# Performance work log

Hardware: AMD Instinct MI355X
Metric: run time of the kernel (lower is better)

## Reference

```python
import jax, jax.numpy as jnp
import numpy as np

# Dims: N tokens, D input, H expert hidden, O output, E experts, G gate hidden, K top-k
N, D, H, O, E, G, K = 8192, 1024, 2048, 1024, 8, 256, 2
BALANCE_COEF = 0.01


def setup_inputs() -> dict:
    key = jax.random.key(0)
    ks = jax.random.split(key, 12)
    def lin(k, shape, fan_in):
        return jax.random.normal(k, shape, jnp.float32) * (1.0 / np.sqrt(fan_in))
    return {
        "x":   jax.random.normal(ks[0], (N, D), jnp.float32),
        # gating MLP: D -> G -> E
        "Wg1": lin(ks[1], (D, G), D), "bg1": jnp.zeros((G,), jnp.float32),
        "Wg2": lin(ks[2], (G, E), G), "bg2": jnp.zeros((E,), jnp.float32),
        # stacked expert MLPs: D -> H -> H -> O (ExpertNetwork, num_layers=2)
        "W1": lin(ks[3], (E, D, H), D), "b1": jnp.zeros((E, H), jnp.float32),
        "W2": lin(ks[4], (E, H, H), H), "b2": jnp.zeros((E, H), jnp.float32),
        "W3": lin(ks[5], (E, H, O), H), "b3": jnp.zeros((E, O), jnp.float32),
    }


def reference(x, Wg1, bg1, Wg2, bg2, W1, b1, W2, b2, W3, b3):
    # Gating: 2-layer MLP -> softmax -> top-k -> renormalize (eval: no noise/dropout)
    logits = jnp.maximum(x @ Wg1 + bg1, 0.0) @ Wg2 + bg2            # [N, E]
    probs = jax.nn.softmax(logits, axis=-1)
    w, idx = jax.lax.top_k(probs, K)                                # [N, K]
    w = w / jnp.sum(w, axis=-1, keepdims=True)
    onehot = jax.nn.one_hot(idx, E, dtype=x.dtype)                  # [N, K, E]
    comb = jnp.sum(onehot * w[..., None], axis=1)                   # [N, E] per-token expert weight

    # Dense-equivalent combine: unselected tokens get weight 0, identical math to
    # the masked dispatch + scatter-add in the torch code.
    def expert_step(acc, params):
        W1e, b1e, W2e, b2e, W3e, b3e, we = params                   # we: [N]
        h = jnp.maximum(x @ W1e + b1e, 0.0)                         # [N, H]
        h = jnp.maximum(h @ W2e + b2e, 0.0)                         # [N, H]
        o = h @ W3e + b3e                                           # [N, O]
        return acc + o * we[:, None], None

    out, _ = jax.lax.scan(expert_step, jnp.zeros((N, O), x.dtype),
                          (W1, b1, W2, b2, W3, b3, comb.T))

    # aux losses: expert_usage[e] = sum_i mean_b(indices[b,i]==e)
    expert_usage = jnp.sum(onehot, axis=(0, 1)) / N                 # [E]
    balance_loss = jnp.mean((expert_usage - 1.0 / E) ** 2) * BALANCE_COEF
    return out, balance_loss, expert_usage
```

## Files before the change

### kernel.cpp

```cpp
#include <hip/hip_runtime.h>
#include <hip/hip_bf16.h>
#include <cstdint>
#include <cstddef>

#define N_TOK 8192
#define D_IN  1024
#define H_DIM 2048
#define O_DIM 1024
#define E_NUM 8
#define G_DIM 256
#define MAXTILES 136
#define MAXROWS  (MAXTILES*128)

typedef __attribute__((ext_vector_type(8))) __bf16 bf16x8;
typedef __attribute__((ext_vector_type(4))) __bf16 bf16x4;
typedef __attribute__((ext_vector_type(4))) float floatx4;

#define GCAST(p) ((__attribute__((address_space(1))) void*)(void*)(p))
#define LCAST(p) ((__attribute__((address_space(3))) void*)(p))

#define JOB_G1_END   512
#define JOB_CAST_END 4608
#define JOB_W1_END   8704
#define JOB_W2_END   16896
#define JOB_W3_END   20992

__device__ inline void transpose_body(const float* __restrict__ src,
                                      __bf16* __restrict__ dst,
                                      int K, int N, int e, int ktile, int ntile,
                                      float* smemf) {
  float (*tl)[68] = (float(*)[68])smemf;
  const float* s = src + (size_t)e * K * N;
  __bf16* d = dst + (size_t)e * K * N;
  int k0 = ktile * 64, n0 = ntile * 64;
  int t = threadIdx.x;
  int kr = t >> 4, nc = t & 15;
#pragma unroll
  for (int p = 0; p < 4; p++) {
    float4 v = *reinterpret_cast<const float4*>(
        s + (size_t)(k0 + kr + p * 16) * N + n0 + nc * 4);
    *reinterpret_cast<float4*>(&tl[kr + p * 16][nc * 4]) = v;
  }
  __syncthreads();
  int n = t >> 2, kg = t & 3;
#pragma unroll
  for (int p = 0; p < 2; p++) {
    bf16x8 o;
#pragma unroll
    for (int j = 0; j < 8; j++) o[j] = (__bf16)tl[p * 32 + kg * 8 + j][n];
    *reinterpret_cast<bf16x8*>(d + (size_t)(n0 + n) * K + k0 + p * 32 + kg * 8) = o;
  }
}

__device__ inline void gate1_body(const float* __restrict__ x,
                                  const float* __restrict__ Wg1,
                                  const float* __restrict__ bg1,
                                  float* __restrict__ g,
                                  int bn, int bm, float* smemf) {
  float (*As)[68] = (float(*)[68])smemf;
  float (*Bs)[68] = (float(*)[68])(smemf + 32 * 68);
  int t = threadIdx.x;
  int tm = t >> 4, tn = t & 15;
  float acc[4][4] = {};
  for (int k0 = 0; k0 < D_IN; k0 += 32) {
#pragma unroll
    for (int i = 0; i < 2; i++) {
      int idx = t + 256 * i;
      int row = idx >> 3, c4 = idx & 7;
      float4 v = *reinterpret_cast<const float4*>(
          x + (size_t)(bm * 64 + row) * D_IN + k0 + c4 * 4);
      As[c4 * 4 + 0][row] = v.x;
      As[c4 * 4 + 1][row] = v.y;
      As[c4 * 4 + 2][row] = v.z;
      As[c4 * 4 + 3][row] = v.w;
      int brow = idx >> 4, bc4 = idx & 15;
      float4 wv = *reinterpret_cast<const float4*>(
          Wg1 + (size_t)(k0 + brow) * G_DIM + bn * 64 + bc4 * 4);
      *reinterpret_cast<float4*>(&Bs[brow][bc4 * 4]) = wv;
    }
    __syncthreads();
#pragma unroll
    for (int k = 0; k < 32; k++) {
      float4 av = *reinterpret_cast<const float4*>(&As[k][tm * 4]);
      float4 bv = *reinterpret_cast<const float4*>(&Bs[k][tn * 4]);
      float a4[4] = {av.x, av.y, av.z, av.w};
      float b4[4] = {bv.x, bv.y, bv.z, bv.w};
#pragma unroll
      for (int r = 0; r < 4; r++)
#pragma unroll
        for (int c = 0; c < 4; c++) acc[r][c] = fmaf(a4[r], b4[c], acc[r][c]);
    }
    __syncthreads();
  }
  int gr = bm * 64 + tm * 4, gc = bn * 64 + tn * 4;
#pragma unroll
  for (int r = 0; r < 4; r++) {
    float4 o;
    o.x = fmaxf(acc[r][0] + bg1[gc + 0], 0.f);
    o.y = fmaxf(acc[r][1] + bg1[gc + 1], 0.f);
    o.z = fmaxf(acc[r][2] + bg1[gc + 2], 0.f);
    o.w = fmaxf(acc[r][3] + bg1[gc + 3], 0.f);
    *reinterpret_cast<float4*>(g + (size_t)(gr + r) * G_DIM + gc) = o;
  }
}

__global__ __launch_bounds__(256) void prep_kernel(
    const float* __restrict__ x, __bf16* __restrict__ xb,
    const float* __restrict__ W1, __bf16* __restrict__ W1t,
    const float* __restrict__ W2, __bf16* __restrict__ W2t,
    const float* __restrict__ W3, __bf16* __restrict__ W3t,
    const float* __restrict__ Wg1, const float* __restrict__ bg1,
    float* __restrict__ g) {
  __shared__ float smemf[4352];
  int b = blockIdx.x;
  if (b < JOB_G1_END) {
    gate1_body(x, Wg1, bg1, g, b & 3, b >> 2, smemf);
  } else if (b < JOB_CAST_END) {
    int id = b - JOB_G1_END;
    int i = id * 2048 + threadIdx.x * 8;
    float4 v0 = *reinterpret_cast<const float4*>(x + i);
    float4 v1 = *reinterpret_cast<const float4*>(x + i + 4);
    bf16x8 o;
    o[0] = (__bf16)v0.x; o[1] = (__bf16)v0.y; o[2] = (__bf16)v0.z; o[3] = (__bf16)v0.w;
    o[4] = (__bf16)v1.x; o[5] = (__bf16)v1.y; o[6] = (__bf16)v1.z; o[7] = (__bf16)v1.w;
    *reinterpret_cast<bf16x8*>(xb + i) = o;
  } else if (b < JOB_W1_END) {
    int id = b - JOB_CAST_END;
    transpose_body(W1, W1t, D_IN, H_DIM, id >> 9, (id >> 5) & 15, id & 31, smemf);
  } else if (b < JOB_W2_END) {
    int id = b - JOB_W1_END;
    transpose_body(W2, W2t, H_DIM, H_DIM, id >> 10, (id >> 5) & 31, id & 31, smemf);
  } else {
    int id = b - JOB_W2_END;
    transpose_body(W3, W3t, H_DIM, O_DIM, id >> 9, (id >> 4) & 31, id & 15, smemf);
  }
}

__global__ __launch_bounds__(256) void gate2_kernel(const float* __restrict__ g,
                                                    const float* __restrict__ Wg2,
                                                    const float* __restrict__ bg2,
                                                    int* __restrict__ top_idx,
                                                    float* __restrict__ top_w,
                                                    int* __restrict__ counts) {
  __shared__ float lg[32][9];
  int t = threadIdx.x;
  int tl = t >> 3, e = t & 7;
  int n = blockIdx.x * 32 + tl;
  const float* gr = g + (size_t)n * G_DIM;
  float acc = bg2[e];
  for (int i = 0; i < G_DIM; i += 4) {
    float4 v = *reinterpret_cast<const float4*>(gr + i);
    acc += v.x * Wg2[(i + 0) * E_NUM + e];
    acc += v.y * Wg2[(i + 1) * E_NUM + e];
    acc += v.z * Wg2[(i + 2) * E_NUM + e];
    acc += v.w * Wg2[(i + 3) * E_NUM + e];
  }
  lg[tl][e] = acc;
  __syncthreads();
  if (e == 0) {
    float l[8];
#pragma unroll
    for (int i = 0; i < 8; i++) l[i] = lg[tl][i];
    int i0 = 0;
    for (int i = 1; i < 8; i++)
      if (l[i] > l[i0]) i0 = i;
    int i1 = (i0 == 0) ? 1 : 0;
    for (int i = 0; i < 8; i++)
      if (i != i0 && l[i] > l[i1]) i1 = i;
    float d = expf(l[i1] - l[i0]);
    float w0 = 1.f / (1.f + d);
    float w1 = d * w0;
    top_idx[n * 2 + 0] = i0;
    top_idx[n * 2 + 1] = i1;
    top_w[n * 2 + 0] = w0;
    top_w[n * 2 + 1] = w1;
    atomicAdd(&counts[i0], 1);
    atomicAdd(&counts[i1], 1);
  }
}

__global__ void g3_kernel(const int* __restrict__ counts, int* __restrict__ cursors,
                          int* __restrict__ off_pad, int* __restrict__ ntiles,
                          int* __restrict__ tile_meta, float* __restrict__ out_tail,
                          int* __restrict__ slot_token) {
  if (threadIdx.x == 0) {
    int off = 0, nt = 0;
    float mse = 0.f;
    for (int e = 0; e < E_NUM; e++) {
      off_pad[e] = off;
      int c = counts[e];
      int tiles = (c + 127) >> 7;
      for (int i = 0; i < tiles; i++) {
        tile_meta[nt * 2 + 0] = e;
        tile_meta[nt * 2 + 1] = off + i * 128;
        nt++;
      }
      off += tiles << 7;
      cursors[e] = 0;
      float u = (float)c / (float)N_TOK;
      out_tail[1 + e] = u;
      float dd = u - 0.125f;
      mse += dd * dd;
    }
    *ntiles = nt;
    out_tail[0] = (mse / 8.0f) * 0.01f;
  }
  for (int s = threadIdx.x; s < MAXROWS; s += 256) slot_token[s] = 0;
}

__global__ __launch_bounds__(256) void scatter_kernel(const int* __restrict__ top_idx,
                                                      const int* __restrict__ off_pad,
                                                      int* __restrict__ cursors,
                                                      int* __restrict__ slot_token,
                                                      int* __restrict__ token_slots) {
  int n = blockIdx.x * 256 + threadIdx.x;
#pragma unroll
  for (int k = 0; k < 2; k++) {
    int e = top_idx[n * 2 + k];
    int pos = atomicAdd(&cursors[e], 1);
    int s = off_pad[e] + pos;
    slot_token[s] = n;
    token_slots[n * 2 + k] = s;
  }
}

__global__ __launch_bounds__(256) void moe_gemm_kernel(
    const __bf16* __restrict__ A, int Astride, int gatherA,
    const __bf16* __restrict__ Wt, const float* __restrict__ bias,
    int Kdim, int Ndim,
    const int* __restrict__ tile_meta, const int* __restrict__ ntiles_p,
    const int* __restrict__ slot_token,
    __bf16* __restrict__ h_out, float* __restrict__ y_out, int finalMode) {
  int tile = blockIdx.y;
  if (tile >= *ntiles_p) return;
  __shared__ __bf16 As[128 * 32];
  __shared__ __bf16 Bs[128 * 32];
  int ex = tile_meta[tile * 2 + 0];
  int slot0 = tile_meta[tile * 2 + 1];
  int n0 = blockIdx.x * 128;
  int t = threadIdx.x, l = t & 63, w = t >> 6;

  size_t aoff[2], boff[2];
#pragma unroll
  for (int i = 0; i < 2; i++) {
    int gidx = (w * 2 + i) * 64 + l;
    int row = gidx >> 2;
    int kch = (gidx & 3) ^ ((row >> 1) & 3);
    int sl = slot0 + row;
    long long rb = gatherA ? (long long)slot_token[sl] * Astride
                           : (long long)sl * Astride;
    aoff[i] = (size_t)rb + kch * 8;
    boff[i] = ((size_t)ex * Ndim + n0 + row) * (size_t)Kdim + kch * 8;
  }

  int wm = (w >> 1) * 64, wn = (w & 1) * 64;
  int lm = l & 15, lq = l >> 4;
  floatx4 acc[4][4] = {};

  for (int k0 = 0; k0 < Kdim; k0 += 32) {
#pragma unroll
    for (int i = 0; i < 2; i++) {
      __builtin_amdgcn_global_load_lds(GCAST(A + aoff[i] + k0),
                                       LCAST((char*)As + w * 2048 + i * 1024),
                                       16, 0, 0);
      __builtin_amdgcn_global_load_lds(GCAST(Wt + boff[i] + k0),
                                       LCAST((char*)Bs + w * 2048 + i * 1024),
                                       16, 0, 0);
    }
    __syncthreads();
    bf16x8 af[4], bfr[4];
#pragma unroll
    for (int i = 0; i < 4; i++) {
      int r = wm + i * 16 + lm;
      int s = lq ^ ((r >> 1) & 3);
      af[i] = *reinterpret_cast<const bf16x8*>(As + r * 32 + s * 8);
    }
#pragma unroll
    for (int j = 0; j < 4; j++) {
      int r = wn + j * 16 + lm;
      int s = lq ^ ((r >> 1) & 3);
      bfr[j] = *reinterpret_cast<const bf16x8*>(Bs + r * 32 + s * 8);
    }
#pragma unroll
    for (int i = 0; i < 4; i++)
#pragma unroll
      for (int j = 0; j < 4; j++)
        acc[i][j] = __builtin_amdgcn_mfma_f32_16x16x32_bf16(af[i], bfr[j], acc[i][j], 0, 0, 0);
    __syncthreads();
  }

  float bcol[4];
#pragma unroll
  for (int j = 0; j < 4; j++) bcol[j] = bias[(size_t)ex * Ndim + n0 + wn + j * 16 + lm];

  if (finalMode) {
#pragma unroll
    for (int i = 0; i < 4; i++) {
#pragma unroll
      for (int r = 0; r < 4; r++) {
        int sl = slot0 + wm + i * 16 + lq * 4 + r;
        float* yrow = y_out + (size_t)sl * Ndim + n0 + wn + lm;
#pragma unroll
        for (int j = 0; j < 4; j++) yrow[j * 16] = acc[i][j][r] + bcol[j];
      }
    }
  } else {
#pragma unroll
    for (int i = 0; i < 4; i++) {
#pragma unroll
      for (int r = 0; r < 4; r++) {
        int sl = slot0 + wm + i * 16 + lq * 4 + r;
        __bf16* hrow = h_out + (size_t)sl * Ndim + n0 + wn + lm;
#pragma unroll
        for (int j = 0; j < 4; j++) {
          float v = fmaxf(acc[i][j][r] + bcol[j], 0.f);
          hrow[j * 16] = (__bf16)v;
        }
      }
    }
  }
}

__global__ __launch_bounds__(256) void combine_kernel(const float* __restrict__ y,
                                                      const int* __restrict__ token_slots,
                                                      const float* __restrict__ top_w,
                                                      float* __restrict__ out) {
  int n = blockIdx.x;
  int t = threadIdx.x;
  int s0 = token_slots[n * 2 + 0], s1 = token_slots[n * 2 + 1];
  float w0 = top_w[n * 2 + 0], w1 = top_w[n * 2 + 1];
  float4 a = reinterpret_cast<const float4*>(y + (size_t)s0 * O_DIM)[t];
  float4 b = reinterpret_cast<const float4*>(y + (size_t)s1 * O_DIM)[t];
  float4 o;
  o.x = w0 * a.x + w1 * b.x;
  o.y = w0 * a.y + w1 * b.y;
  o.z = w0 * a.z + w1 * b.z;
  o.w = w0 * a.w + w1 * b.w;
  reinterpret_cast<float4*>(out + (size_t)n * O_DIM)[t] = o;
}

extern "C" void kernel_launch(void* const* d_in, const int* in_sizes, int n_in,
                              void* d_out, int out_size, void* d_ws, size_t ws_size,
                              hipStream_t stream) {
  const float* x   = (const float*)d_in[0];
  const float* Wg1 = (const float*)d_in[1];
  const float* bg1 = (const float*)d_in[2];
  const float* Wg2 = (const float*)d_in[3];
  const float* bg2 = (const float*)d_in[4];
  const float* W1  = (const float*)d_in[5];
  const float* b1  = (const float*)d_in[6];
  const float* W2  = (const float*)d_in[7];
  const float* b2  = (const float*)d_in[8];
  const float* W3  = (const float*)d_in[9];
  const float* b3  = (const float*)d_in[10];
  float* out = (float*)d_out;

  char* ws = (char*)d_ws;
  __bf16* x_bf       = (__bf16*)(ws + 0);
  __bf16* W1t        = (__bf16*)(ws + 16777216);
  __bf16* W2t        = (__bf16*)(ws + 50331648);
  __bf16* W3t        = (__bf16*)(ws + 117440512);
  __bf16* h1         = (__bf16*)(ws + 150994944);
  __bf16* h2         = (__bf16*)(ws + 222298112);
  float*  y          = (float*) (ws + 150994944);
  float*  gbuf       = (float*) (ws + 293601280);
  int*    top_idx    = (int*)   (ws + 301989888);
  float*  top_w      = (float*) (ws + 302055424);
  int*    slot_token = (int*)   (ws + 302120960);
  int*    token_slots= (int*)   (ws + 302190592);
  int*    meta       = (int*)   (ws + 302260224);
  int* counts    = meta;
  int* cursors   = meta + 8;
  int* off_pad   = meta + 16;
  int* ntiles    = meta + 24;
  int* tile_meta = meta + 32;
  float* out_tail = out + (size_t)N_TOK * O_DIM;

  hipMemsetAsync(meta, 0, 64, stream);

  prep_kernel<<<JOB_W3_END, 256, 0, stream>>>(x, x_bf, W1, W1t, W2, W2t, W3, W3t,
                                              Wg1, bg1, gbuf);
  gate2_kernel<<<N_TOK / 32, 256, 0, stream>>>(gbuf, Wg2, bg2, top_idx, top_w, counts);
  g3_kernel<<<1, 256, 0, stream>>>(counts, cursors, off_pad, ntiles, tile_meta, out_tail,
                                   slot_token);
  scatter_kernel<<<N_TOK / 256, 256, 0, stream>>>(top_idx, off_pad, cursors,
                                                  slot_token, token_slots);

  moe_gemm_kernel<<<dim3(H_DIM / 128, MAXTILES), 256, 0, stream>>>(
      x_bf, D_IN, 1, W1t, b1, D_IN, H_DIM, tile_meta, ntiles, slot_token,
      h1, nullptr, 0);
  moe_gemm_kernel<<<dim3(H_DIM / 128, MAXTILES), 256, 0, stream>>>(
      h1, H_DIM, 0, W2t, b2, H_DIM, H_DIM, tile_meta, ntiles, slot_token,
      h2, nullptr, 0);
  moe_gemm_kernel<<<dim3(O_DIM / 128, MAXTILES), 256, 0, stream>>>(
      h2, H_DIM, 0, W3t, b3, H_DIM, O_DIM, tile_meta, ntiles, slot_token,
      nullptr, y, 1);
  combine_kernel<<<N_TOK, 256, 0, stream>>>(y, token_slots, top_w, out);
}
```

Measured before the change: 1.006 ms.

## Overlap W2/W3 transposes with first expert GEMM, deepen K tile to 64

Moves the W2 and W3 fp32-to-bf16 transposes out of the prep kernel and into extra blocks of the first expert GEMM launch, so that conversion work runs alongside the W1 GEMM instead of ahead of it. The GEMM K step doubles from 32 to 64 with a matching 8-way XOR swizzle in LDS, halving the barrier count per tile. The transpose scratch drops its padding and uses an XOR-style rotation to avoid bank conflicts instead. This raises LDS use to 32KB per block, which may lower occupancy, and the W1 GEMM launch grows by many extra blocks.

```diff
diff --git a/kernel.cpp b/kernel.cpp
--- a/kernel.cpp
+++ b/kernel.cpp
@@ -13,7 +13,6 @@
 #define MAXROWS  (MAXTILES*128)
 
 typedef __attribute__((ext_vector_type(8))) __bf16 bf16x8;
-typedef __attribute__((ext_vector_type(4))) __bf16 bf16x4;
 typedef __attribute__((ext_vector_type(4))) float floatx4;
 
 #define GCAST(p) ((__attribute__((address_space(1))) void*)(void*)(p))
@@ -22,14 +21,12 @@
 #define JOB_G1_END   512
 #define JOB_CAST_END 4608
 #define JOB_W1_END   8704
-#define JOB_W2_END   16896
-#define JOB_W3_END   20992
 
 __device__ inline void transpose_body(const float* __restrict__ src,
                                       __bf16* __restrict__ dst,
                                       int K, int N, int e, int ktile, int ntile,
                                       float* smemf) {
-  float (*tl)[68] = (float(*)[68])smemf;
+  float (*tl)[64] = (float(*)[64])smemf;
   const float* s = src + (size_t)e * K * N;
   __bf16* d = dst + (size_t)e * K * N;
   int k0 = ktile * 64, n0 = ntile * 64;
@@ -37,18 +34,21 @@
   int kr = t >> 4, nc = t & 15;
 #pragma unroll
   for (int p = 0; p < 4; p++) {
+    int r = kr + p * 16;
     float4 v = *reinterpret_cast<const float4*>(
-        s + (size_t)(k0 + kr + p * 16) * N + n0 + nc * 4);
-    *reinterpret_cast<float4*>(&tl[kr + p * 16][nc * 4]) = v;
+        s + (size_t)(k0 + r) * N + n0 + nc * 4);
+    *reinterpret_cast<float4*>(&tl[r][(nc * 4 + 8 * (r >> 3)) & 63]) = v;
   }
   __syncthreads();
-  int n = t >> 2, kg = t & 3;
+  int n = t >> 3, kg = t & 7;
 #pragma unroll
   for (int p = 0; p < 2; p++) {
+    int c = n + p * 32;
     bf16x8 o;
 #pragma unroll
-    for (int j = 0; j < 8; j++) o[j] = (__bf16)tl[p * 32 + kg * 8 + j][n];
-    *reinterpret_cast<bf16x8*>(d + (size_t)(n0 + n) * K + k0 + p * 32 + kg * 8) = o;
+    for (int j = 0; j < 8; j++)
+      o[j] = (__bf16)tl[kg * 8 + j][(c + 8 * kg) & 63];
+    *reinterpret_cast<bf16x8*>(d + (size_t)(n0 + c) * K + k0 + kg * 8) = o;
   }
 }
 
@@ -107,8 +107,6 @@
 __global__ __launch_bounds__(256) void prep_kernel(
     const float* __restrict__ x, __bf16* __restrict__ xb,
     const float* __restrict__ W1, __bf16* __restrict__ W1t,
-    const float* __restrict__ W2, __bf16* __restrict__ W2t,
-    const float* __restrict__ W3, __bf16* __restrict__ W3t,
     const float* __restrict__ Wg1, const float* __restrict__ bg1,
     float* __restrict__ g) {
   __shared__ float smemf[4352];
@@ -124,15 +122,9 @@
     o[0] = (__bf16)v0.x; o[1] = (__bf16)v0.y; o[2] = (__bf16)v0.z; o[3] = (__bf16)v0.w;
     o[4] = (__bf16)v1.x; o[5] = (__bf16)v1.y; o[6] = (__bf16)v1.z; o[7] = (__bf16)v1.w;
     *reinterpret_cast<bf16x8*>(xb + i) = o;
-  } else if (b < JOB_W1_END) {
+  } else {
     int id = b - JOB_CAST_END;
     transpose_body(W1, W1t, D_IN, H_DIM, id >> 9, (id >> 5) & 15, id & 31, smemf);
-  } else if (b < JOB_W2_END) {
-    int id = b - JOB_W1_END;
-    transpose_body(W2, W2t, H_DIM, H_DIM, id >> 10, (id >> 5) & 31, id & 31, smemf);
-  } else {
-    int id = b - JOB_W2_END;
-    transpose_body(W3, W3t, H_DIM, O_DIM, id >> 9, (id >> 4) & 31, id & 15, smemf);
   }
 }
 
@@ -230,22 +222,37 @@
     int Kdim, int Ndim,
     const int* __restrict__ tile_meta, const int* __restrict__ ntiles_p,
     const int* __restrict__ slot_token,
-    __bf16* __restrict__ h_out, float* __restrict__ y_out, int finalMode) {
+    __bf16* __restrict__ h_out, float* __restrict__ y_out, int finalMode,
+    const float* __restrict__ W2src, __bf16* __restrict__ W2dst,
+    const float* __restrict__ W3src, __bf16* __restrict__ W3dst) {
+  __shared__ __align__(16) char smem[32768];
   int tile = blockIdx.y;
+  if (tile >= MAXTILES) {
+    int id = (tile - MAXTILES) * gridDim.x + blockIdx.x;
+    if (id < 8192) {
+      transpose_body(W2src, W2dst, H_DIM, H_DIM, id >> 10, (id >> 5) & 31,
+                     id & 31, (float*)smem);
+    } else {
+      id -= 8192;
+      transpose_body(W3src, W3dst, H_DIM, O_DIM, id >> 9, (id >> 4) & 31,
+                     id & 15, (float*)smem);
+    }
+    return;
+  }
   if (tile >= *ntiles_p) return;
-  __shared__ __bf16 As[128 * 32];
-  __shared__ __bf16 Bs[128 * 32];
+  __bf16* As = (__bf16*)smem;
+  __bf16* Bs = (__bf16*)(smem + 16384);
   int ex = tile_meta[tile * 2 + 0];
   int slot0 = tile_meta[tile * 2 + 1];
   int n0 = blockIdx.x * 128;
   int t = threadIdx.x, l = t & 63, w = t >> 6;
 
-  size_t aoff[2], boff[2];
-#pragma unroll
-  for (int i = 0; i < 2; i++) {
-    int gidx = (w * 2 + i) * 64 + l;
-    int row = gidx >> 2;
-    int kch = (gidx & 3) ^ ((row >> 1) & 3);
+  size_t aoff[4], boff[4];
+#pragma unroll
+  for (int i = 0; i < 4; i++) {
+    int gidx = (w * 4 + i) * 64 + l;
+    int row = gidx >> 3;
+    int kch = (gidx & 7) ^ (row & 7);
     int sl = slot0 + row;
     long long rb = gatherA ? (long long)slot_token[sl] * Astride
                            : (long long)sl * Astride;
@@ -257,35 +264,39 @@
   int lm = l & 15, lq = l >> 4;
   floatx4 acc[4][4] = {};
 
-  for (int k0 = 0; k0 < Kdim; k0 += 32) {
-#pragma unroll
-    for (int i = 0; i < 2; i++) {
+  for (int k0 = 0; k0 < Kdim; k0 += 64) {
+#pragma unroll
+    for (int i = 0; i < 4; i++) {
       __builtin_amdgcn_global_load_lds(GCAST(A + aoff[i] + k0),
-                                       LCAST((char*)As + w * 2048 + i * 1024),
+                                       LCAST((char*)As + w * 4096 + i * 1024),
                                        16, 0, 0);
       __builtin_amdgcn_global_load_lds(GCAST(Wt + boff[i] + k0),
-                                       LCAST((char*)Bs + w * 2048 + i * 1024),
+                                       LCAST((char*)Bs + w * 4096 + i * 1024),
                                        16, 0, 0);
     }
     __syncthreads();
-    bf16x8 af[4], bfr[4];
-#pragma unroll
-    for (int i = 0; i < 4; i++) {
-      int r = wm + i * 16 + lm;
-      int s = lq ^ ((r >> 1) & 3);
-      af[i] = *reinterpret_cast<const bf16x8*>(As + r * 32 + s * 8);
-    }
-#pragma unroll
-    for (int j = 0; j < 4; j++) {
-      int r = wn + j * 16 + lm;
-      int s = lq ^ ((r >> 1) & 3);
-      bfr[j] = *reinterpret_cast<const bf16x8*>(Bs + r * 32 + s * 8);
-    }
-#pragma unroll
-    for (int i = 0; i < 4; i++)
-#pragma unroll
-      for (int j = 0; j < 4; j++)
-        acc[i][j] = __builtin_amdgcn_mfma_f32_16x16x32_bf16(af[i], bfr[j], acc[i][j], 0, 0, 0);
+#pragma unroll
+    for (int half = 0; half < 2; half++) {
+      bf16x8 af[4], bfr[4];
+#pragma unroll
+      for (int i = 0; i < 4; i++) {
+        int r = wm + i * 16 + lm;
+        int s = (half * 4 + lq) ^ (r & 7);
+        af[i] = *reinterpret_cast<const bf16x8*>(As + r * 64 + s * 8);
+      }
+#pragma unroll
+      for (int j = 0; j < 4; j++) {
+        int r = wn + j * 16 + lm;
+        int s = (half * 4 + lq) ^ (r & 7);
+        bfr[j] = *reinterpret_cast<const bf16x8*>(Bs + r * 64 + s * 8);
+      }
+#pragma unroll
+      for (int i = 0; i < 4; i++)
+#pragma unroll
+        for (int j = 0; j < 4; j++)
+          acc[i][j] = __builtin_amdgcn_mfma_f32_16x16x32_bf16(af[i], bfr[j],
+                                                              acc[i][j], 0, 0, 0);
+    }
     __syncthreads();
   }
 
@@ -378,22 +389,21 @@
 
   hipMemsetAsync(meta, 0, 64, stream);
 
-  prep_kernel<<<JOB_W3_END, 256, 0, stream>>>(x, x_bf, W1, W1t, W2, W2t, W3, W3t,
-                                              Wg1, bg1, gbuf);
+  prep_kernel<<<JOB_W1_END, 256, 0, stream>>>(x, x_bf, W1, W1t, Wg1, bg1, gbuf);
   gate2_kernel<<<N_TOK / 32, 256, 0, stream>>>(gbuf, Wg2, bg2, top_idx, top_w, counts);
   g3_kernel<<<1, 256, 0, stream>>>(counts, cursors, off_pad, ntiles, tile_meta, out_tail,
                                    slot_token);
   scatter_kernel<<<N_TOK / 256, 256, 0, stream>>>(top_idx, off_pad, cursors,
                                                   slot_token, token_slots);
 
-  moe_gemm_kernel<<<dim3(H_DIM / 128, MAXTILES), 256, 0, stream>>>(
+  moe_gemm_kernel<<<dim3(H_DIM / 128, MAXTILES + 768), 256, 0, stream>>>(
       x_bf, D_IN, 1, W1t, b1, D_IN, H_DIM, tile_meta, ntiles, slot_token,
-      h1, nullptr, 0);
+      h1, nullptr, 0, W2, W2t, W3, W3t);
   moe_gemm_kernel<<<dim3(H_DIM / 128, MAXTILES), 256, 0, stream>>>(
       h1, H_DIM, 0, W2t, b2, H_DIM, H_DIM, tile_meta, ntiles, slot_token,
-      h2, nullptr, 0);
+      h2, nullptr, 0, nullptr, nullptr, nullptr, nullptr);
   moe_gemm_kernel<<<dim3(O_DIM / 128, MAXTILES), 256, 0, stream>>>(
       h2, H_DIM, 0, W3t, b3, H_DIM, O_DIM, tile_meta, ntiles, slot_token,
-      nullptr, y, 1);
+      nullptr, y, 1, nullptr, nullptr, nullptr, nullptr);
   combine_kernel<<<N_TOK, 256, 0, stream>>>(y, token_slots, top_w, out);
 }
```

Measured after the change: 944.6 us, median of 2. 1.06x faster.
